# Performance work log

Hardware: AMD Instinct MI355X
Metric: run time of the kernel (lower is better)

## Reference

```python
import jax, jax.numpy as jnp
import numpy as np

N, M, FIN, FOUT, E = 8, 50000, 32, 32, 800000


def setup_inputs() -> dict:
    key = jax.random.key(0)
    ks = jax.random.split(key, 6)
    x = jax.random.normal(ks[0], (N, M, FIN), dtype=jnp.float32)
    adj_rows = jax.random.randint(ks[1], (E,), 0, M, dtype=jnp.int32)
    adj_cols = jax.random.randint(ks[2], (E,), 0, M, dtype=jnp.int32)
    adj_vals = jax.random.uniform(ks[3], (E,), dtype=jnp.float32)
    stdv = 1.0 / np.sqrt(FOUT)
    weight = jax.random.uniform(ks[4], (FIN, FOUT), dtype=jnp.float32, minval=-stdv, maxval=stdv)
    bias = jax.random.uniform(ks[5], (FOUT,), dtype=jnp.float32, minval=-stdv, maxval=stdv)
    return {"x": x, "adj_rows": adj_rows, "adj_cols": adj_cols,
            "adj_vals": adj_vals, "weight": weight, "bias": bias}


def reference(x, adj_rows, adj_cols, adj_vals, weight, bias):
    # spmm(adj, x) over the node axis M for every batch element.
    # adj is COO: out[:, r, :] += v * x[:, c, :] for each edge (r, c, v).
    xe = jnp.take(x, adj_cols, axis=1) * adj_vals[None, :, None]  # [N, E, Fin]
    y = jnp.zeros_like(x).at[:, adj_rows, :].add(xe)              # [N, M, Fin]
    # dense linear + bias: (N*M, Fin) @ (Fin, Fout) + bias
    return jnp.einsum('nmf,fo->nmo', y, weight) + bias
```

## Files before the change

### kernel.cpp

```cpp
#include <hip/hip_runtime.h>
#include <hip/hip_bf16.h>

#define NB 8
#define MN 50000
#define FI 32
#define FO 32
#define NE 800000
#define CAPLOG 6
#define CAP 64
#define NBINS 196
#define BINCAPLOG 13

__global__ __launch_bounds__(256) void gemm_xw(const float* __restrict__ x,
                                               const float* __restrict__ W,
                                               unsigned int* __restrict__ zb,
                                               int* __restrict__ gCursor) {
    int bid = blockIdx.x;
    int t   = threadIdx.x;

    if (bid == 0 && t < NBINS) gCursor[t] = t << BINCAPLOG;

    __shared__ float Ws[FI * FO];
    ((float4*)Ws)[t] = ((const float4*)W)[t];
    __syncthreads();

    int n     = bid / 3125;
    int mb    = bid % 3125;
    int rowid = t >> 4;
    int j     = t & 15;
    int m     = mb * 16 + rowid;

    const float4* xr = (const float4*)(x + ((long)n * MN + m) * FI);
    float4 xv[8];
#pragma unroll
    for (int i = 0; i < 8; ++i) xv[i] = xr[i];
    const float* xf = (const float*)xv;

    float a0 = 0.f, a1 = 0.f;
#pragma unroll
    for (int k = 0; k < FI; ++k) {
        a0 += xf[k] * Ws[k * FO + 2 * j];
        a1 += xf[k] * Ws[k * FO + 2 * j + 1];
    }
    unsigned int lo = (unsigned int)__bfloat16_as_ushort(__float2bfloat16(a0));
    unsigned int hi = (unsigned int)__bfloat16_as_ushort(__float2bfloat16(a1));
    zb[(long)m * 128 + n * 16 + j] = lo | (hi << 16);
}

__global__ __launch_bounds__(256) void bin_edges(const int* __restrict__ rows,
                                                 const int* __restrict__ cols,
                                                 const float* __restrict__ vals,
                                                 int* __restrict__ gCursor,
                                                 unsigned long long* __restrict__ sorted) {
    __shared__ int cnt[NBINS];
    __shared__ int base[NBINS];
    int t = threadIdx.x;
    for (int i = t; i < NBINS; i += 256) cnt[i] = 0;
    __syncthreads();

    unsigned long long pk[8];
    int bn[8], rk[8];
    int e0 = blockIdx.x * 2048;
#pragma unroll
    for (int k = 0; k < 8; ++k) {
        int e = e0 + k * 256 + t;
        bn[k] = -1;
        if (e < NE) {
            int r = rows[e];
            unsigned int vb = (unsigned int)__bfloat16_as_ushort(__float2bfloat16(vals[e]));
            pk[k] = ((unsigned long long)(unsigned int)r << 32) |
                    (unsigned long long)((vb << 16) | (unsigned int)cols[e]);
            bn[k] = r >> 8;
            rk[k] = atomicAdd(&cnt[bn[k]], 1);
        }
    }
    __syncthreads();
    if (t < NBINS) base[t] = atomicAdd(&gCursor[t], cnt[t]);
    __syncthreads();
#pragma unroll
    for (int k = 0; k < 8; ++k) {
        if (bn[k] >= 0) {
            int pos = base[bn[k]] + rk[k];
            if (pos < ((bn[k] + 1) << BINCAPLOG))
                sorted[pos] = pk[k];
        }
    }
}

__global__ __launch_bounds__(1024) void fill_sorted(const unsigned long long* __restrict__ sorted,
                                                    const int* __restrict__ gCursor,
                                                    unsigned int* __restrict__ bucket,
                                                    int* __restrict__ cursor) {
    __shared__ int cur[256];
    int t   = threadIdx.x;
    int bin = blockIdx.x;
    if (t < 256) cur[t] = 0;
    __syncthreads();

    int beg = bin << BINCAPLOG;
    int cnt = gCursor[bin] - beg;
    if (cnt > (1 << BINCAPLOG)) cnt = (1 << BINCAPLOG);

    for (int i = t; i < cnt; i += 1024) {
        unsigned long long pk = sorted[beg + i];
        int r  = (int)(pk >> 32);
        int lr = r & 255;
        int p  = atomicAdd(&cur[lr], 1);
        if (p < CAP)
            bucket[((long)r << CAPLOG) + p] = (unsigned int)pk;
    }
    __syncthreads();
    if (t < 256) {
        int R = (bin << 8) + t;
        if (R < MN) cursor[R] = cur[t] > CAP ? CAP : cur[t];
    }
}

__global__ __launch_bounds__(256) void aggregate(const unsigned long long* __restrict__ zb2,
                                                 const int* __restrict__ cursor,
                                                 const unsigned int* __restrict__ bucket,
                                                 const float* __restrict__ bias,
                                                 float4* __restrict__ out4) {
    int lane = threadIdx.x & 63;
    int r    = blockIdx.x * 4 + (threadIdx.x >> 6);

    int cnt = cursor[r];
    cnt = cnt > CAP ? CAP : cnt;

    unsigned int mypk = bucket[(r << CAPLOG) + lane];

    int n  = lane >> 3;
    int fp = lane & 7;
    float4 acc = ((const float4*)bias)[fp];

    int i = 0;
    for (; i + 8 <= cnt; i += 8) {
        unsigned int pk[8];
        unsigned long long z[8];
#pragma unroll
        for (int k = 0; k < 8; ++k) pk[k] = __shfl(mypk, i + k);
#pragma unroll
        for (int k = 0; k < 8; ++k) z[k] = zb2[((long)(pk[k] & 0xffff) << 6) + lane];
#pragma unroll
        for (int k = 0; k < 8; ++k) {
            float v = __uint_as_float(pk[k] & 0xffff0000u);
            unsigned int l = (unsigned int)z[k], h = (unsigned int)(z[k] >> 32);
            acc.x += v * __uint_as_float(l << 16);
            acc.y += v * __uint_as_float(l & 0xffff0000u);
            acc.z += v * __uint_as_float(h << 16);
            acc.w += v * __uint_as_float(h & 0xffff0000u);
        }
    }
    for (; i + 4 <= cnt; i += 4) {
        unsigned int pk[4];
        unsigned long long z[4];
#pragma unroll
        for (int k = 0; k < 4; ++k) pk[k] = __shfl(mypk, i + k);
#pragma unroll
        for (int k = 0; k < 4; ++k) z[k] = zb2[((long)(pk[k] & 0xffff) << 6) + lane];
#pragma unroll
        for (int k = 0; k < 4; ++k) {
            float v = __uint_as_float(pk[k] & 0xffff0000u);
            unsigned int l = (unsigned int)z[k], h = (unsigned int)(z[k] >> 32);
            acc.x += v * __uint_as_float(l << 16);
            acc.y += v * __uint_as_float(l & 0xffff0000u);
            acc.z += v * __uint_as_float(h << 16);
            acc.w += v * __uint_as_float(h & 0xffff0000u);
        }
    }
    for (; i < cnt; ++i) {
        unsigned int p0 = __shfl(mypk, i);
        float v0 = __uint_as_float(p0 & 0xffff0000u);
        unsigned long long z0 = zb2[((long)(p0 & 0xffff) << 6) + lane];
        unsigned int l0 = (unsigned int)z0, h0 = (unsigned int)(z0 >> 32);
        acc.x += v0 * __uint_as_float(l0 << 16);
        acc.y += v0 * __uint_as_float(l0 & 0xffff0000u);
        acc.z += v0 * __uint_as_float(h0 << 16);
        acc.w += v0 * __uint_as_float(h0 & 0xffff0000u);
    }

    out4[((long)n * MN + r) * 8 + fp] = acc;
}

extern "C" void kernel_launch(void* const* d_in, const int* in_sizes, int n_in,
                              void* d_out, int out_size, void* d_ws, size_t ws_size,
                              hipStream_t stream) {
    const float* x    = (const float*)d_in[0];
    const int*   rows = (const int*)d_in[1];
    const int*   cols = (const int*)d_in[2];
    const float* vals = (const float*)d_in[3];
    const float* W    = (const float*)d_in[4];
    const float* bias = (const float*)d_in[5];
    float4* out4 = (float4*)d_out;

    char* ws = (char*)d_ws;
    size_t off_z      = 0;
    size_t off_cursor = off_z + (size_t)MN * NB * FO * 2;
    size_t off_gcur   = off_cursor + (size_t)MN * 4;
    size_t off_bucket = off_gcur + 1024;
    size_t off_sorted = off_bucket + (size_t)MN * CAP * 4;

    unsigned int*       zb      = (unsigned int*)(ws + off_z);
    int*                cursor  = (int*)(ws + off_cursor);
    int*                gCursor = (int*)(ws + off_gcur);
    unsigned int*       bucket  = (unsigned int*)(ws + off_bucket);
    unsigned long long* sorted  = (unsigned long long*)(ws + off_sorted);

    gemm_xw<<<25000, 256, 0, stream>>>(x, W, zb, gCursor);

    bin_edges<<<392, 256, 0, stream>>>(rows, cols, vals, gCursor, sorted);

    fill_sorted<<<NBINS, 1024, 0, stream>>>(sorted, gCursor, bucket, cursor);

    aggregate<<<MN / 4, 256, 0, stream>>>((const unsigned long long*)zb, cursor, bucket,
                                          bias, out4);
}
```

Measured before the change: 120.2 us.

## Fuse edge binning into GEMM prep kernel and add nontemporal loads/stores

Merges the bin_edges and gemm_xw kernels into one launch: the first 392 blocks bin edges and the rest compute the bf16 X·W product. The bin cursors are now relative offsets zeroed by a memset instead of being initialised inside the GEMM kernel. Streaming reads of x, rows, cols and vals use nontemporal loads, and the output store is nontemporal. The aim is to drop a kernel launch and a serialization point so binning overlaps with the GEMM. In exchange it adds a memset node and mixes two very different block types in one grid.

```diff
diff --git a/kernel.cpp b/kernel.cpp
--- a/kernel.cpp
+++ b/kernel.cpp
@@ -10,30 +10,74 @@
 #define CAP 64
 #define NBINS 196
 #define BINCAPLOG 13
-
-__global__ __launch_bounds__(256) void gemm_xw(const float* __restrict__ x,
-                                               const float* __restrict__ W,
-                                               unsigned int* __restrict__ zb,
-                                               int* __restrict__ gCursor) {
+#define BIN_BLOCKS 392
+
+typedef float f32x4 __attribute__((ext_vector_type(4)));
+
+__global__ __launch_bounds__(256) void fused_prep(const float* __restrict__ x,
+                                                  const float* __restrict__ W,
+                                                  const int* __restrict__ rows,
+                                                  const int* __restrict__ cols,
+                                                  const float* __restrict__ vals,
+                                                  int* __restrict__ gCursor,
+                                                  unsigned long long* __restrict__ sorted,
+                                                  unsigned int* __restrict__ zb) {
     int bid = blockIdx.x;
     int t   = threadIdx.x;
 
-    if (bid == 0 && t < NBINS) gCursor[t] = t << BINCAPLOG;
+    if (bid < BIN_BLOCKS) {
+        __shared__ int cnt[NBINS];
+        __shared__ int base[NBINS];
+        for (int i = t; i < NBINS; i += 256) cnt[i] = 0;
+        __syncthreads();
+
+        unsigned long long pk[8];
+        int bn[8], rk[8];
+        int e0 = bid * 2048;
+#pragma unroll
+        for (int k = 0; k < 8; ++k) {
+            int e = e0 + k * 256 + t;
+            bn[k] = -1;
+            if (e < NE) {
+                int r = __builtin_nontemporal_load(&rows[e]);
+                int c = __builtin_nontemporal_load(&cols[e]);
+                float vf = __builtin_nontemporal_load(&vals[e]);
+                unsigned int vb = (unsigned int)__bfloat16_as_ushort(__float2bfloat16(vf));
+                pk[k] = ((unsigned long long)(unsigned int)r << 32) |
+                        (unsigned long long)((vb << 16) | (unsigned int)c);
+                bn[k] = r >> 8;
+                rk[k] = atomicAdd(&cnt[bn[k]], 1);
+            }
+        }
+        __syncthreads();
+        if (t < NBINS) base[t] = atomicAdd(&gCursor[t], cnt[t]);
+        __syncthreads();
+#pragma unroll
+        for (int k = 0; k < 8; ++k) {
+            if (bn[k] >= 0) {
+                int rel = base[bn[k]] + rk[k];
+                if (rel < (1 << BINCAPLOG))
+                    sorted[(bn[k] << BINCAPLOG) + rel] = pk[k];
+            }
+        }
+        return;
+    }
 
     __shared__ float Ws[FI * FO];
     ((float4*)Ws)[t] = ((const float4*)W)[t];
     __syncthreads();
 
-    int n     = bid / 3125;
-    int mb    = bid % 3125;
+    int gb    = bid - BIN_BLOCKS;
+    int n     = gb / 3125;
+    int mb    = gb % 3125;
     int rowid = t >> 4;
     int j     = t & 15;
     int m     = mb * 16 + rowid;
 
-    const float4* xr = (const float4*)(x + ((long)n * MN + m) * FI);
-    float4 xv[8];
-#pragma unroll
-    for (int i = 0; i < 8; ++i) xv[i] = xr[i];
+    const f32x4* xr = (const f32x4*)(x + ((long)n * MN + m) * FI);
+    f32x4 xv[8];
+#pragma unroll
+    for (int i = 0; i < 8; ++i) xv[i] = __builtin_nontemporal_load(&xr[i]);
     const float* xf = (const float*)xv;
 
     float a0 = 0.f, a1 = 0.f;
@@ -45,46 +89,6 @@
     unsigned int lo = (unsigned int)__bfloat16_as_ushort(__float2bfloat16(a0));
     unsigned int hi = (unsigned int)__bfloat16_as_ushort(__float2bfloat16(a1));
     zb[(long)m * 128 + n * 16 + j] = lo | (hi << 16);
-}
-
-__global__ __launch_bounds__(256) void bin_edges(const int* __restrict__ rows,
-                                                 const int* __restrict__ cols,
-                                                 const float* __restrict__ vals,
-                                                 int* __restrict__ gCursor,
-                                                 unsigned long long* __restrict__ sorted) {
-    __shared__ int cnt[NBINS];
-    __shared__ int base[NBINS];
-    int t = threadIdx.x;
-    for (int i = t; i < NBINS; i += 256) cnt[i] = 0;
-    __syncthreads();
-
-    unsigned long long pk[8];
-    int bn[8], rk[8];
-    int e0 = blockIdx.x * 2048;
-#pragma unroll
-    for (int k = 0; k < 8; ++k) {
-        int e = e0 + k * 256 + t;
-        bn[k] = -1;
-        if (e < NE) {
-            int r = rows[e];
-            unsigned int vb = (unsigned int)__bfloat16_as_ushort(__float2bfloat16(vals[e]));
-            pk[k] = ((unsigned long long)(unsigned int)r << 32) |
-                    (unsigned long long)((vb << 16) | (unsigned int)cols[e]);
-            bn[k] = r >> 8;
-            rk[k] = atomicAdd(&cnt[bn[k]], 1);
-        }
-    }
-    __syncthreads();
-    if (t < NBINS) base[t] = atomicAdd(&gCursor[t], cnt[t]);
-    __syncthreads();
-#pragma unroll
-    for (int k = 0; k < 8; ++k) {
-        if (bn[k] >= 0) {
-            int pos = base[bn[k]] + rk[k];
-            if (pos < ((bn[k] + 1) << BINCAPLOG))
-                sorted[pos] = pk[k];
-        }
-    }
 }
 
 __global__ __launch_bounds__(1024) void fill_sorted(const unsigned long long* __restrict__ sorted,
@@ -98,7 +102,7 @@
     __syncthreads();
 
     int beg = bin << BINCAPLOG;
-    int cnt = gCursor[bin] - beg;
+    int cnt = gCursor[bin];
     if (cnt > (1 << BINCAPLOG)) cnt = (1 << BINCAPLOG);
 
     for (int i = t; i < cnt; i += 1024) {
@@ -120,7 +124,7 @@
                                                  const int* __restrict__ cursor,
                                                  const unsigned int* __restrict__ bucket,
                                                  const float* __restrict__ bias,
-                                                 float4* __restrict__ out4) {
+                                                 f32x4* __restrict__ out4) {
     int lane = threadIdx.x & 63;
     int r    = blockIdx.x * 4 + (threadIdx.x >> 6);
 
@@ -131,7 +135,8 @@
 
     int n  = lane >> 3;
     int fp = lane & 7;
-    float4 acc = ((const float4*)bias)[fp];
+    float4 b4 = ((const float4*)bias)[fp];
+    f32x4 acc = {b4.x, b4.y, b4.z, b4.w};
 
     int i = 0;
     for (; i + 8 <= cnt; i += 8) {
@@ -179,7 +184,7 @@
         acc.w += v0 * __uint_as_float(h0 & 0xffff0000u);
     }
 
-    out4[((long)n * MN + r) * 8 + fp] = acc;
+    __builtin_nontemporal_store(acc, &out4[((long)n * MN + r) * 8 + fp]);
 }
 
 extern "C" void kernel_launch(void* const* d_in, const int* in_sizes, int n_in,
@@ -191,7 +196,7 @@
     const float* vals = (const float*)d_in[3];
     const float* W    = (const float*)d_in[4];
     const float* bias = (const float*)d_in[5];
-    float4* out4 = (float4*)d_out;
+    f32x4* out4 = (f32x4*)d_out;
 
     char* ws = (char*)d_ws;
     size_t off_z      = 0;
@@ -206,9 +211,10 @@
     unsigned int*       bucket  = (unsigned int*)(ws + off_bucket);
     unsigned long long* sorted  = (unsigned long long*)(ws + off_sorted);
 
-    gemm_xw<<<25000, 256, 0, stream>>>(x, W, zb, gCursor);
-
-    bin_edges<<<392, 256, 0, stream>>>(rows, cols, vals, gCursor, sorted);
+    (void)hipMemsetAsync(gCursor, 0, NBINS * 4, stream);
+
+    fused_prep<<<BIN_BLOCKS + 25000, 256, 0, stream>>>(x, W, rows, cols, vals,
+                                                       gCursor, sorted, zb);
 
     fill_sorted<<<NBINS, 1024, 0, stream>>>(sorted, gCursor, bucket, cursor);
 
```

New measurement: 135.2 us. 1.12x slower.

## Fuse bucket fill into aggregation using LDS buckets with smaller 64-row bins

Applied to the files above, without the earlier changes.

Merges the fill_sorted and aggregate kernels: each 1024-thread block takes a 64-row bin, builds the per-row edge buckets in shared memory, then sums over them directly. This removes the global bucket and cursor arrays, their write and reread, and one kernel launch. Bins shrink from 256 to 64 rows (782 bins, 2048-entry capacity each), and outputs use nontemporal stores. The trade-off is fewer, larger blocks for the gather phase (782 blocks of 16 waves, 4 rows per wave), which may limit latency hiding. Rows whose bin overflows the smaller per-bin capacity also lose edges silently.

```diff
diff --git a/kernel.cpp b/kernel.cpp
--- a/kernel.cpp
+++ b/kernel.cpp
@@ -8,8 +8,13 @@
 #define NE 800000
 #define CAPLOG 6
 #define CAP 64
-#define NBINS 196
-#define BINCAPLOG 13
+#define BINSHIFT 6
+#define BINROWS 64
+#define NBINS 782
+#define BINCAPLOG 11
+#define BIN_BLOCKS 392
+
+typedef float f32x4 __attribute__((ext_vector_type(4)));
 
 __global__ __launch_bounds__(256) void gemm_xw(const float* __restrict__ x,
                                                const float* __restrict__ W,
@@ -18,7 +23,9 @@
     int bid = blockIdx.x;
     int t   = threadIdx.x;
 
-    if (bid == 0 && t < NBINS) gCursor[t] = t << BINCAPLOG;
+    if (bid == 0) {
+        for (int i = t; i < NBINS; i += 256) gCursor[i] = i << BINCAPLOG;
+    }
 
     __shared__ float Ws[FI * FO];
     ((float4*)Ws)[t] = ((const float4*)W)[t];
@@ -70,12 +77,12 @@
             unsigned int vb = (unsigned int)__bfloat16_as_ushort(__float2bfloat16(vals[e]));
             pk[k] = ((unsigned long long)(unsigned int)r << 32) |
                     (unsigned long long)((vb << 16) | (unsigned int)cols[e]);
-            bn[k] = r >> 8;
+            bn[k] = r >> BINSHIFT;
             rk[k] = atomicAdd(&cnt[bn[k]], 1);
         }
     }
     __syncthreads();
-    if (t < NBINS) base[t] = atomicAdd(&gCursor[t], cnt[t]);
+    for (int i = t; i < NBINS; i += 256) base[i] = atomicAdd(&gCursor[i], cnt[i]);
     __syncthreads();
 #pragma unroll
     for (int k = 0; k < 8; ++k) {
@@ -87,14 +94,16 @@
     }
 }
 
-__global__ __launch_bounds__(1024) void fill_sorted(const unsigned long long* __restrict__ sorted,
-                                                    const int* __restrict__ gCursor,
-                                                    unsigned int* __restrict__ bucket,
-                                                    int* __restrict__ cursor) {
-    __shared__ int cur[256];
+__global__ __launch_bounds__(1024) void agg_fused(const unsigned long long* __restrict__ zb2,
+                                                  const int* __restrict__ gCursor,
+                                                  const unsigned long long* __restrict__ sorted,
+                                                  const float* __restrict__ bias,
+                                                  f32x4* __restrict__ out4) {
+    __shared__ unsigned int lbkt[BINROWS * CAP];
+    __shared__ int lcur[BINROWS];
     int t   = threadIdx.x;
     int bin = blockIdx.x;
-    if (t < 256) cur[t] = 0;
+    if (t < BINROWS) lcur[t] = 0;
     __syncthreads();
 
     int beg = bin << BINCAPLOG;
@@ -103,83 +112,78 @@
 
     for (int i = t; i < cnt; i += 1024) {
         unsigned long long pk = sorted[beg + i];
-        int r  = (int)(pk >> 32);
-        int lr = r & 255;
-        int p  = atomicAdd(&cur[lr], 1);
+        int lr = ((int)(pk >> 32)) & (BINROWS - 1);
+        int p  = atomicAdd(&lcur[lr], 1);
         if (p < CAP)
-            bucket[((long)r << CAPLOG) + p] = (unsigned int)pk;
-    }
-    __syncthreads();
-    if (t < 256) {
-        int R = (bin << 8) + t;
-        if (R < MN) cursor[R] = cur[t] > CAP ? CAP : cur[t];
-    }
-}
-
-__global__ __launch_bounds__(256) void aggregate(const unsigned long long* __restrict__ zb2,
-                                                 const int* __restrict__ cursor,
-                                                 const unsigned int* __restrict__ bucket,
-                                                 const float* __restrict__ bias,
-                                                 float4* __restrict__ out4) {
-    int lane = threadIdx.x & 63;
-    int r    = blockIdx.x * 4 + (threadIdx.x >> 6);
-
-    int cnt = cursor[r];
-    cnt = cnt > CAP ? CAP : cnt;
-
-    unsigned int mypk = bucket[(r << CAPLOG) + lane];
-
-    int n  = lane >> 3;
-    int fp = lane & 7;
-    float4 acc = ((const float4*)bias)[fp];
-
-    int i = 0;
-    for (; i + 8 <= cnt; i += 8) {
-        unsigned int pk[8];
-        unsigned long long z[8];
-#pragma unroll
-        for (int k = 0; k < 8; ++k) pk[k] = __shfl(mypk, i + k);
-#pragma unroll
-        for (int k = 0; k < 8; ++k) z[k] = zb2[((long)(pk[k] & 0xffff) << 6) + lane];
-#pragma unroll
-        for (int k = 0; k < 8; ++k) {
-            float v = __uint_as_float(pk[k] & 0xffff0000u);
-            unsigned int l = (unsigned int)z[k], h = (unsigned int)(z[k] >> 32);
-            acc.x += v * __uint_as_float(l << 16);
-            acc.y += v * __uint_as_float(l & 0xffff0000u);
-            acc.z += v * __uint_as_float(h << 16);
-            acc.w += v * __uint_as_float(h & 0xffff0000u);
-        }
-    }
-    for (; i + 4 <= cnt; i += 4) {
-        unsigned int pk[4];
-        unsigned long long z[4];
-#pragma unroll
-        for (int k = 0; k < 4; ++k) pk[k] = __shfl(mypk, i + k);
-#pragma unroll
-        for (int k = 0; k < 4; ++k) z[k] = zb2[((long)(pk[k] & 0xffff) << 6) + lane];
-#pragma unroll
-        for (int k = 0; k < 4; ++k) {
-            float v = __uint_as_float(pk[k] & 0xffff0000u);
-            unsigned int l = (unsigned int)z[k], h = (unsigned int)(z[k] >> 32);
-            acc.x += v * __uint_as_float(l << 16);
-            acc.y += v * __uint_as_float(l & 0xffff0000u);
-            acc.z += v * __uint_as_float(h << 16);
-            acc.w += v * __uint_as_float(h & 0xffff0000u);
-        }
-    }
-    for (; i < cnt; ++i) {
-        unsigned int p0 = __shfl(mypk, i);
-        float v0 = __uint_as_float(p0 & 0xffff0000u);
-        unsigned long long z0 = zb2[((long)(p0 & 0xffff) << 6) + lane];
-        unsigned int l0 = (unsigned int)z0, h0 = (unsigned int)(z0 >> 32);
-        acc.x += v0 * __uint_as_float(l0 << 16);
-        acc.y += v0 * __uint_as_float(l0 & 0xffff0000u);
-        acc.z += v0 * __uint_as_float(h0 << 16);
-        acc.w += v0 * __uint_as_float(h0 & 0xffff0000u);
-    }
-
-    out4[((long)n * MN + r) * 8 + fp] = acc;
+            lbkt[(lr << CAPLOG) + p] = (unsigned int)pk;
+    }
+    __syncthreads();
+
+    int lane = t & 63;
+    int w    = t >> 6;
+    int n    = lane >> 3;
+    int fp   = lane & 7;
+    float4 b4 = ((const float4*)bias)[fp];
+
+    for (int q = 0; q < 4; ++q) {
+        int lr = w * 4 + q;
+        int r  = (bin << BINSHIFT) + lr;
+        if (r >= MN) break;
+
+        int cr = lcur[lr];
+        cr = cr > CAP ? CAP : cr;
+        const unsigned int* bp = &lbkt[lr << CAPLOG];
+
+        f32x4 acc = {b4.x, b4.y, b4.z, b4.w};
+
+        int i = 0;
+        for (; i + 8 <= cr; i += 8) {
+            unsigned int pk[8];
+            unsigned long long z[8];
+#pragma unroll
+            for (int k = 0; k < 8; ++k) pk[k] = bp[i + k];
+#pragma unroll
+            for (int k = 0; k < 8; ++k) z[k] = zb2[((long)(pk[k] & 0xffff) << 6) + lane];
+#pragma unroll
+            for (int k = 0; k < 8; ++k) {
+                float v = __uint_as_float(pk[k] & 0xffff0000u);
+                unsigned int l = (unsigned int)z[k], h = (unsigned int)(z[k] >> 32);
+                acc.x += v * __uint_as_float(l << 16);
+                acc.y += v * __uint_as_float(l & 0xffff0000u);
+                acc.z += v * __uint_as_float(h << 16);
+                acc.w += v * __uint_as_float(h & 0xffff0000u);
+            }
+        }
+        for (; i + 4 <= cr; i += 4) {
+            unsigned int pk[4];
+            unsigned long long z[4];
+#pragma unroll
+            for (int k = 0; k < 4; ++k) pk[k] = bp[i + k];
+#pragma unroll
+            for (int k = 0; k < 4; ++k) z[k] = zb2[((long)(pk[k] & 0xffff) << 6) + lane];
+#pragma unroll
+            for (int k = 0; k < 4; ++k) {
+                float v = __uint_as_float(pk[k] & 0xffff0000u);
+                unsigned int l = (unsigned int)z[k], h = (unsigned int)(z[k] >> 32);
+                acc.x += v * __uint_as_float(l << 16);
+                acc.y += v * __uint_as_float(l & 0xffff0000u);
+                acc.z += v * __uint_as_float(h << 16);
+                acc.w += v * __uint_as_float(h & 0xffff0000u);
+            }
+        }
+        for (; i < cr; ++i) {
+            unsigned int p0 = bp[i];
+            float v0 = __uint_as_float(p0 & 0xffff0000u);
+            unsigned long long z0 = zb2[((long)(p0 & 0xffff) << 6) + lane];
+            unsigned int l0 = (unsigned int)z0, h0 = (unsigned int)(z0 >> 32);
+            acc.x += v0 * __uint_as_float(l0 << 16);
+            acc.y += v0 * __uint_as_float(l0 & 0xffff0000u);
+            acc.z += v0 * __uint_as_float(h0 << 16);
+            acc.w += v0 * __uint_as_float(h0 & 0xffff0000u);
+        }
+
+        __builtin_nontemporal_store(acc, &out4[((long)n * MN + r) * 8 + fp]);
+    }
 }
 
 extern "C" void kernel_launch(void* const* d_in, const int* in_sizes, int n_in,
@@ -191,27 +195,21 @@
     const float* vals = (const float*)d_in[3];
     const float* W    = (const float*)d_in[4];
     const float* bias = (const float*)d_in[5];
-    float4* out4 = (float4*)d_out;
+    f32x4* out4 = (f32x4*)d_out;
 
     char* ws = (char*)d_ws;
     size_t off_z      = 0;
-    size_t off_cursor = off_z + (size_t)MN * NB * FO * 2;
-    size_t off_gcur   = off_cursor + (size_t)MN * 4;
-    size_t off_bucket = off_gcur + 1024;
-    size_t off_sorted = off_bucket + (size_t)MN * CAP * 4;
+    size_t off_gcur   = off_z + (size_t)MN * NB * FO * 2;
+    size_t off_sorted = off_gcur + ((size_t)NBINS * 4 + 127 & ~(size_t)127);
 
     unsigned int*       zb      = (unsigned int*)(ws + off_z);
-    int*                cursor  = (int*)(ws + off_cursor);
     int*                gCursor = (int*)(ws + off_gcur);
-    unsigned int*       bucket  = (unsigned int*)(ws + off_bucket);
     unsigned long long* sorted  = (unsigned long long*)(ws + off_sorted);
 
     gemm_xw<<<25000, 256, 0, stream>>>(x, W, zb, gCursor);
 
-    bin_edges<<<392, 256, 0, stream>>>(rows, cols, vals, gCursor, sorted);
-
-    fill_sorted<<<NBINS, 1024, 0, stream>>>(sorted, gCursor, bucket, cursor);
-
-    aggregate<<<MN / 4, 256, 0, stream>>>((const unsigned long long*)zb, cursor, bucket,
-                                          bias, out4);
-}
+    bin_edges<<<BIN_BLOCKS, 256, 0, stream>>>(rows, cols, vals, gCursor, sorted);
+
+    agg_fused<<<NBINS, 1024, 0, stream>>>((const unsigned long long*)zb, gCursor,
+                                          sorted, bias, out4);
+}
```

Measured after the change: 121.1 us. Within noise of the previous version (+0.7%).

## Use 16-byte gathers over two edges per wave and finer edge bins

Applied to the files above, without the earlier changes.

The aggregate kernel now splits each wave into two halves. Each half processes a different edge and gathers 16-byte vectors of the bf16 row, so a wave issues half as many gather instructions, and the two halves are combined with a cross-half shuffle before bias is added and results are stored with nontemporal stores. Edge binning uses 128-row bins (391 bins), which gives fill_sorted more blocks and smaller shared counters. Nontemporal loads are added on the sorted and bucket streams. The cost is an extra reduction shuffle, a more complex odd-count tail, and more global atomics in binning.

```diff
diff --git a/kernel.cpp b/kernel.cpp
--- a/kernel.cpp
+++ b/kernel.cpp
@@ -8,8 +8,14 @@
 #define NE 800000
 #define CAPLOG 6
 #define CAP 64
-#define NBINS 196
-#define BINCAPLOG 13
+#define BINSHIFT 7
+#define BINROWS 128
+#define NBINS 391
+#define BINCAPLOG 12
+#define BIN_BLOCKS 392
+
+typedef float        f32x4 __attribute__((ext_vector_type(4)));
+typedef unsigned int u32x4 __attribute__((ext_vector_type(4)));
 
 __global__ __launch_bounds__(256) void gemm_xw(const float* __restrict__ x,
                                                const float* __restrict__ W,
@@ -18,7 +24,9 @@
     int bid = blockIdx.x;
     int t   = threadIdx.x;
 
-    if (bid == 0 && t < NBINS) gCursor[t] = t << BINCAPLOG;
+    if (bid == 0) {
+        for (int i = t; i < NBINS; i += 256) gCursor[i] = i << BINCAPLOG;
+    }
 
     __shared__ float Ws[FI * FO];
     ((float4*)Ws)[t] = ((const float4*)W)[t];
@@ -70,12 +78,12 @@
             unsigned int vb = (unsigned int)__bfloat16_as_ushort(__float2bfloat16(vals[e]));
             pk[k] = ((unsigned long long)(unsigned int)r << 32) |
                     (unsigned long long)((vb << 16) | (unsigned int)cols[e]);
-            bn[k] = r >> 8;
+            bn[k] = r >> BINSHIFT;
             rk[k] = atomicAdd(&cnt[bn[k]], 1);
         }
     }
     __syncthreads();
-    if (t < NBINS) base[t] = atomicAdd(&gCursor[t], cnt[t]);
+    for (int i = t; i < NBINS; i += 256) base[i] = atomicAdd(&gCursor[i], cnt[i]);
     __syncthreads();
 #pragma unroll
     for (int k = 0; k < 8; ++k) {
@@ -91,10 +99,10 @@
                                                     const int* __restrict__ gCursor,
                                                     unsigned int* __restrict__ bucket,
                                                     int* __restrict__ cursor) {
-    __shared__ int cur[256];
+    __shared__ int cur[BINROWS];
     int t   = threadIdx.x;
     int bin = blockIdx.x;
-    if (t < 256) cur[t] = 0;
+    if (t < BINROWS) cur[t] = 0;
     __syncthreads();
 
     int beg = bin << BINCAPLOG;
@@ -102,84 +110,96 @@
     if (cnt > (1 << BINCAPLOG)) cnt = (1 << BINCAPLOG);
 
     for (int i = t; i < cnt; i += 1024) {
-        unsigned long long pk = sorted[beg + i];
+        unsigned long long pk = __builtin_nontemporal_load(&sorted[beg + i]);
         int r  = (int)(pk >> 32);
-        int lr = r & 255;
+        int lr = r & (BINROWS - 1);
         int p  = atomicAdd(&cur[lr], 1);
         if (p < CAP)
             bucket[((long)r << CAPLOG) + p] = (unsigned int)pk;
     }
     __syncthreads();
-    if (t < 256) {
-        int R = (bin << 8) + t;
+    if (t < BINROWS) {
+        int R = (bin << BINSHIFT) + t;
         if (R < MN) cursor[R] = cur[t] > CAP ? CAP : cur[t];
     }
 }
 
-__global__ __launch_bounds__(256) void aggregate(const unsigned long long* __restrict__ zb2,
+__global__ __launch_bounds__(256) void aggregate(const u32x4* __restrict__ zb4,
                                                  const int* __restrict__ cursor,
                                                  const unsigned int* __restrict__ bucket,
                                                  const float* __restrict__ bias,
-                                                 float4* __restrict__ out4) {
+                                                 f32x4* __restrict__ out4) {
     int lane = threadIdx.x & 63;
     int r    = blockIdx.x * 4 + (threadIdx.x >> 6);
 
     int cnt = cursor[r];
     cnt = cnt > CAP ? CAP : cnt;
 
-    unsigned int mypk = bucket[(r << CAPLOG) + lane];
-
-    int n  = lane >> 3;
-    int fp = lane & 7;
-    float4 acc = ((const float4*)bias)[fp];
+    unsigned int mypk = __builtin_nontemporal_load(&bucket[(r << CAPLOG) + lane]);
+
+    int half = lane >> 5;
+    int sub  = lane & 31;
+
+    float acc[8];
+#pragma unroll
+    for (int k = 0; k < 8; ++k) acc[k] = 0.f;
 
     int i = 0;
     for (; i + 8 <= cnt; i += 8) {
-        unsigned int pk[8];
-        unsigned long long z[8];
-#pragma unroll
-        for (int k = 0; k < 8; ++k) pk[k] = __shfl(mypk, i + k);
-#pragma unroll
-        for (int k = 0; k < 8; ++k) z[k] = zb2[((long)(pk[k] & 0xffff) << 6) + lane];
-#pragma unroll
-        for (int k = 0; k < 8; ++k) {
-            float v = __uint_as_float(pk[k] & 0xffff0000u);
-            unsigned int l = (unsigned int)z[k], h = (unsigned int)(z[k] >> 32);
-            acc.x += v * __uint_as_float(l << 16);
-            acc.y += v * __uint_as_float(l & 0xffff0000u);
-            acc.z += v * __uint_as_float(h << 16);
-            acc.w += v * __uint_as_float(h & 0xffff0000u);
-        }
-    }
-    for (; i + 4 <= cnt; i += 4) {
         unsigned int pk[4];
-        unsigned long long z[4];
-#pragma unroll
-        for (int k = 0; k < 4; ++k) pk[k] = __shfl(mypk, i + k);
-#pragma unroll
-        for (int k = 0; k < 4; ++k) z[k] = zb2[((long)(pk[k] & 0xffff) << 6) + lane];
+        u32x4 zv[4];
+#pragma unroll
+        for (int k = 0; k < 4; ++k) pk[k] = __shfl(mypk, i + 2 * k + half);
+#pragma unroll
+        for (int k = 0; k < 4; ++k) zv[k] = zb4[((long)(pk[k] & 0xffff) << 5) + sub];
 #pragma unroll
         for (int k = 0; k < 4; ++k) {
             float v = __uint_as_float(pk[k] & 0xffff0000u);
-            unsigned int l = (unsigned int)z[k], h = (unsigned int)(z[k] >> 32);
-            acc.x += v * __uint_as_float(l << 16);
-            acc.y += v * __uint_as_float(l & 0xffff0000u);
-            acc.z += v * __uint_as_float(h << 16);
-            acc.w += v * __uint_as_float(h & 0xffff0000u);
-        }
-    }
-    for (; i < cnt; ++i) {
-        unsigned int p0 = __shfl(mypk, i);
-        float v0 = __uint_as_float(p0 & 0xffff0000u);
-        unsigned long long z0 = zb2[((long)(p0 & 0xffff) << 6) + lane];
-        unsigned int l0 = (unsigned int)z0, h0 = (unsigned int)(z0 >> 32);
-        acc.x += v0 * __uint_as_float(l0 << 16);
-        acc.y += v0 * __uint_as_float(l0 & 0xffff0000u);
-        acc.z += v0 * __uint_as_float(h0 << 16);
-        acc.w += v0 * __uint_as_float(h0 & 0xffff0000u);
-    }
-
-    out4[((long)n * MN + r) * 8 + fp] = acc;
+#pragma unroll
+            for (int q = 0; q < 4; ++q) {
+                unsigned int w = zv[k][q];
+                acc[2 * q]     += v * __uint_as_float(w << 16);
+                acc[2 * q + 1] += v * __uint_as_float(w & 0xffff0000u);
+            }
+        }
+    }
+    for (; i + 2 <= cnt; i += 2) {
+        unsigned int pk0 = __shfl(mypk, i + half);
+        u32x4 zv0 = zb4[((long)(pk0 & 0xffff) << 5) + sub];
+        float v = __uint_as_float(pk0 & 0xffff0000u);
+#pragma unroll
+        for (int q = 0; q < 4; ++q) {
+            unsigned int w = zv0[q];
+            acc[2 * q]     += v * __uint_as_float(w << 16);
+            acc[2 * q + 1] += v * __uint_as_float(w & 0xffff0000u);
+        }
+    }
+    if (i < cnt) {
+        unsigned int pk0 = __shfl(mypk, i);
+        int   c = (half == 0) ? (int)(pk0 & 0xffff) : 0;
+        float v = (half == 0) ? __uint_as_float(pk0 & 0xffff0000u) : 0.f;
+        u32x4 zv0 = zb4[((long)c << 5) + sub];
+#pragma unroll
+        for (int q = 0; q < 4; ++q) {
+            unsigned int w = zv0[q];
+            acc[2 * q]     += v * __uint_as_float(w << 16);
+            acc[2 * q + 1] += v * __uint_as_float(w & 0xffff0000u);
+        }
+    }
+
+#pragma unroll
+    for (int k = 0; k < 8; ++k) acc[k] += __shfl_xor(acc[k], 32);
+
+    if (half == 0) {
+        int n  = sub >> 2;
+        int j4 = sub & 3;
+        const float* bb = bias + j4 * 8;
+        f32x4 o0 = {acc[0] + bb[0], acc[1] + bb[1], acc[2] + bb[2], acc[3] + bb[3]};
+        f32x4 o1 = {acc[4] + bb[4], acc[5] + bb[5], acc[6] + bb[6], acc[7] + bb[7]};
+        long ob = ((long)n * MN + r) * 8 + j4 * 2;
+        __builtin_nontemporal_store(o0, &out4[ob]);
+        __builtin_nontemporal_store(o1, &out4[ob + 1]);
+    }
 }
 
 extern "C" void kernel_launch(void* const* d_in, const int* in_sizes, int n_in,
@@ -191,13 +211,13 @@
     const float* vals = (const float*)d_in[3];
     const float* W    = (const float*)d_in[4];
     const float* bias = (const float*)d_in[5];
-    float4* out4 = (float4*)d_out;
+    f32x4* out4 = (f32x4*)d_out;
 
     char* ws = (char*)d_ws;
     size_t off_z      = 0;
     size_t off_cursor = off_z + (size_t)MN * NB * FO * 2;
     size_t off_gcur   = off_cursor + (size_t)MN * 4;
-    size_t off_bucket = off_gcur + 1024;
+    size_t off_bucket = off_gcur + (((size_t)NBINS * 4 + 127) & ~(size_t)127);
     size_t off_sorted = off_bucket + (size_t)MN * CAP * 4;
 
     unsigned int*       zb      = (unsigned int*)(ws + off_z);
@@ -208,10 +228,9 @@
 
     gemm_xw<<<25000, 256, 0, stream>>>(x, W, zb, gCursor);
 
-    bin_edges<<<392, 256, 0, stream>>>(rows, cols, vals, gCursor, sorted);
+    bin_edges<<<BIN_BLOCKS, 256, 0, stream>>>(rows, cols, vals, gCursor, sorted);
 
     fill_sorted<<<NBINS, 1024, 0, stream>>>(sorted, gCursor, bucket, cursor);
 
-    aggregate<<<MN / 4, 256, 0, stream>>>((const unsigned long long*)zb, cursor, bucket,
-                                          bias, out4);
-}
+    aggregate<<<MN / 4, 256, 0, stream>>>((const u32x4*)zb, cursor, bucket, bias, out4);
+}
```

Measured after the change: 119.8 us. About the same (-0.3%).
